# Performance work log

Measured on AMD Instinct MI355X. Metric: run time of the kernel, lower is better.

The kernel has to match this reference:

```python
import jax, jax.numpy as jnp
import numpy as np

B, N = 8192, 4096
OUT_DIM = 32


def setup_inputs() -> dict:
    key = jax.random.key(0)
    k_rr, k_drop, k_w1, k_b1, k_w2, k_b2 = jax.random.split(key, 6)
    rr = jax.random.uniform(k_rr, (B, N), dtype=jnp.float32, minval=0.4, maxval=1.4)
    drop = jax.random.uniform(k_drop, (B, N)) < 0.3
    rr = jnp.where(drop, 0.0, rr)
    # projection MLP params (Linear(6,16) -> ReLU -> Dropout(eval: identity) -> Linear(16,32))
    w1 = jax.random.normal(k_w1, (6, 16), dtype=jnp.float32) * (1.0 / np.sqrt(6))
    b1 = jax.random.normal(k_b1, (16,), dtype=jnp.float32) * 0.01
    w2 = jax.random.normal(k_w2, (16, OUT_DIM), dtype=jnp.float32) * (1.0 / np.sqrt(16))
    b2 = jax.random.normal(k_b2, (OUT_DIM,), dtype=jnp.float32) * 0.01
    return {"rr_intervals": rr, "w1": w1, "b1": b1, "w2": w2, "b2": b2}


def _hrv_features(rr):
    # rr: (B, N) float32, zero-padded. Faithful to the per-row torch loop, vectorized.
    dt = rr.dtype
    mask = rr > 0                                   # (B, N)
    cnt = jnp.sum(mask, axis=1)                     # (B,) int
    cntf = cnt.astype(dt)
    # masked mean / unbiased std (torch.std default ddof=1)
    denom_m = jnp.maximum(cntf, 1.0)
    mean_rr = jnp.sum(jnp.where(mask, rr, 0.0), axis=1) / denom_m
    dev = jnp.where(mask, rr - mean_rr[:, None], 0.0)
    var = jnp.sum(dev * dev, axis=1) / jnp.maximum(cntf - 1.0, 1.0)
    sdnn = jnp.sqrt(var)
    # compact valid entries to the front (stable -> preserves order), so diffs
    # match torch.diff(rr[rr > 0])
    order = jnp.argsort(jnp.logical_not(mask), axis=1, stable=True)  # (B, N)
    compact = jnp.take_along_axis(rr, order, axis=1)                  # (B, N)
    diffs = compact[:, 1:] - compact[:, :-1]                          # (B, N-1)
    dmask = jnp.arange(N - 1)[None, :] < (cnt - 1)[:, None]           # valid diffs
    ndiff = jnp.maximum(cntf - 1.0, 1.0)
    rmssd = jnp.sqrt(jnp.sum(jnp.where(dmask, diffs * diffs, 0.0), axis=1) / ndiff)
    nn50 = jnp.sum(((jnp.abs(diffs) > 0.05) & dmask).astype(dt), axis=1)
    pnn50 = nn50 / ndiff
    hr = 60.0 / jnp.maximum(mean_rr, 1e-12)
    cv = sdnn / jnp.maximum(mean_rr, 1e-12)
    feats = jnp.stack([mean_rr, sdnn, rmssd, pnn50, hr, cv], axis=1)  # (B, 6)
    feats = jnp.where((cnt > 1)[:, None], feats, 0.0)
    # per-column batch normalization, applied only where column max > 0
    col_max = jnp.max(feats, axis=0)
    col_mean = jnp.mean(feats, axis=0)
    col_std = jnp.std(feats, axis=0, ddof=1)
    normed = (feats - col_mean[None, :]) / (col_std[None, :] + 1e-8)
    feats = jnp.where((col_max > 0)[None, :], normed, feats)
    return feats


def reference(rr_intervals, w1, b1, w2, b2):
    feats = _hrv_features(rr_intervals)                 # (B, 6)
    h = jax.nn.relu(feats @ w1 + b1)                    # (B, 16); dropout in eval = identity
    return h @ w2 + b2                                  # (B, OUT_DIM)
```

## Files before the change

kernel.cpp:

```cpp
#include <hip/hip_runtime.h>
#include <math.h>

#define BATCH 8192
#define NLEN 4096

__global__ __launch_bounds__(256) void hrv_feats_kernel(
    const float* __restrict__ rr, float* __restrict__ feats) {
    const int lane = threadIdx.x & 63;
    const int wid = threadIdx.x >> 6;
    const int row = blockIdx.x * 4 + wid;
    const float* r = rr + (size_t)row * NLEN + lane * 64;

    double dsum = 0.0, dsumsq = 0.0, dsumd2 = 0.0;
    int cnt = 0, nn50 = 0;
    float prev = 0.f, first = 0.f;
    bool has = false;

    float x[32];
    float4* xv = reinterpret_cast<float4*>(x);
    const float4* rv = reinterpret_cast<const float4*>(r);

#pragma unroll
    for (int half = 0; half < 2; ++half) {
#pragma unroll
        for (int i = 0; i < 8; ++i) xv[i] = rv[half * 8 + i];
#pragma unroll
        for (int c = 0; c < 2; ++c) {
            float s = 0.f, s2 = 0.f, d2 = 0.f;
#pragma unroll
            for (int i = 0; i < 16; ++i) {
                const float v = x[c * 16 + i];
                const bool valid = v > 0.f;
                s += v;
                s2 = fmaf(v, v, s2);
                cnt += valid ? 1 : 0;
                const float d = v - prev;
                const float dm = (valid && has) ? d : 0.f;
                d2 = fmaf(dm, dm, d2);
                nn50 += (fabsf(dm) > 0.05f) ? 1 : 0;
                first = (valid && !has) ? v : first;
                prev = valid ? v : prev;
                has = has || valid;
            }
            dsum += s;
            dsumsq += s2;
            dsumd2 += d2;
        }
    }

    unsigned long long m = __ballot(has);
    unsigned long long pm = m & ((1ull << lane) - 1ull);
    int j = 63 - __clzll(pm | 1ull);
    float lastj = __shfl(prev, j, 64);
    if (has && pm) {
        float d = first - lastj;
        dsumd2 += (double)(d * d);
        nn50 += (fabsf(d) > 0.05f) ? 1 : 0;
    }

#pragma unroll
    for (int off = 32; off; off >>= 1) {
        dsum += __shfl_xor(dsum, off, 64);
        dsumsq += __shfl_xor(dsumsq, off, 64);
        dsumd2 += __shfl_xor(dsumd2, off, 64);
        cnt += __shfl_xor(cnt, off, 64);
        nn50 += __shfl_xor(nn50, off, 64);
    }

    const float cntf = (float)cnt;
    const float denom_m = fmaxf(cntf, 1.f);
    const float mean = (float)(dsum / (double)denom_m);
    const float varsum = (float)(dsumsq - (double)cnt * (double)mean * (double)mean);
    const float denom_v = fmaxf(cntf - 1.f, 1.f);
    const float sdnn = sqrtf(fmaxf(varsum / denom_v, 0.f));
    const float rmssd = sqrtf(fmaxf((float)(dsumd2 / (double)denom_v), 0.f));
    const float pnn50 = (float)nn50 / denom_v;
    const float hr = 60.f / fmaxf(mean, 1e-12f);
    const float cv = sdnn / fmaxf(mean, 1e-12f);

    float val = mean;
    val = (lane == 1) ? sdnn : val;
    val = (lane == 2) ? rmssd : val;
    val = (lane == 3) ? pnn50 : val;
    val = (lane == 4) ? hr : val;
    val = (lane == 5) ? cv : val;
    if (cnt <= 1) val = 0.f;
    if (lane < 6) feats[lane * BATCH + row] = val;
}

__global__ __launch_bounds__(256) void stats_mlp_kernel(
    const float* __restrict__ feats,
    const float* __restrict__ w1, const float* __restrict__ b1,
    const float* __restrict__ w2, const float* __restrict__ b2,
    float* __restrict__ out) {
    __shared__ double sh_s[4][6], sh_s2[4][6];
    __shared__ float sh_m[4][6];
    __shared__ float sh_stats[18];

    const int t = threadIdx.x;
    double s[6], s2[6];
    float mx[6];
#pragma unroll
    for (int c = 0; c < 6; ++c) { s[c] = 0.0; s2[c] = 0.0; mx[c] = -INFINITY; }

#pragma unroll
    for (int c = 0; c < 6; ++c) {
        const float4* col = reinterpret_cast<const float4*>(feats + c * BATCH);
#pragma unroll
        for (int it = 0; it < BATCH / 4 / 256; ++it) {
            float4 f4 = col[t + it * 256];
            const float f[4] = {f4.x, f4.y, f4.z, f4.w};
#pragma unroll
            for (int k = 0; k < 4; ++k) {
                s[c] += (double)f[k];
                s2[c] += (double)f[k] * (double)f[k];
                mx[c] = fmaxf(mx[c], f[k]);
            }
        }
    }
#pragma unroll
    for (int off = 32; off; off >>= 1) {
#pragma unroll
        for (int c = 0; c < 6; ++c) {
            s[c] += __shfl_down(s[c], off, 64);
            s2[c] += __shfl_down(s2[c], off, 64);
            mx[c] = fmaxf(mx[c], __shfl_down(mx[c], off, 64));
        }
    }
    if ((t & 63) == 0) {
        const int w = t >> 6;
#pragma unroll
        for (int c = 0; c < 6; ++c) {
            sh_s[w][c] = s[c];
            sh_s2[w][c] = s2[c];
            sh_m[w][c] = mx[c];
        }
    }
    __syncthreads();
    if (t < 6) {
        double S = 0, S2 = 0;
        float M = -INFINITY;
        for (int w = 0; w < 4; ++w) {
            S += sh_s[w][t];
            S2 += sh_s2[w][t];
            M = fmaxf(M, sh_m[w][t]);
        }
        const double meanb = S / (double)BATCH;
        double var = (S2 - (double)BATCH * meanb * meanb) / (double)(BATCH - 1);
        if (var < 0.0) var = 0.0;
        sh_stats[t] = (float)meanb;
        sh_stats[6 + t] = (float)sqrt(var);
        sh_stats[12 + t] = M;
    }
    __syncthreads();

    const int row = blockIdx.x * 256 + t;
    float f[6];
#pragma unroll
    for (int c = 0; c < 6; ++c) {
        float v = feats[c * BATCH + row];
        if (sh_stats[12 + c] > 0.f) v = (v - sh_stats[c]) / (sh_stats[6 + c] + 1e-8f);
        f[c] = v;
    }
    float h[16];
#pragma unroll
    for (int j = 0; j < 16; ++j) {
        float a = b1[j];
#pragma unroll
        for (int c = 0; c < 6; ++c) a = fmaf(f[c], w1[c * 16 + j], a);
        h[j] = fmaxf(a, 0.f);
    }
    float o[32];
#pragma unroll
    for (int k = 0; k < 32; ++k) o[k] = b2[k];
#pragma unroll
    for (int j = 0; j < 16; ++j) {
        const float hj = h[j];
#pragma unroll
        for (int k = 0; k < 32; ++k) o[k] = fmaf(hj, w2[j * 32 + k], o[k]);
    }
    float4* ov = reinterpret_cast<float4*>(out + (size_t)row * 32);
    const float4* op = reinterpret_cast<const float4*>(o);
#pragma unroll
    for (int i = 0; i < 8; ++i) ov[i] = op[i];
}

extern "C" void kernel_launch(void* const* d_in, const int* in_sizes, int n_in,
                              void* d_out, int out_size, void* d_ws, size_t ws_size,
                              hipStream_t stream) {
    const float* rr = (const float*)d_in[0];
    const float* w1 = (const float*)d_in[1];
    const float* b1 = (const float*)d_in[2];
    const float* w2 = (const float*)d_in[3];
    const float* b2 = (const float*)d_in[4];
    float* out = (float*)d_out;
    float* feats = (float*)d_ws;

    hrv_feats_kernel<<<BATCH / 4, 256, 0, stream>>>(rr, feats);
    stats_mlp_kernel<<<BATCH / 256, 256, 0, stream>>>(feats, w1, b1, w2, b2, out);
}
```

Measured before the change: 42.54 us.

## Coalesce row loads by interleaving float4 chunks across lanes with segmented boundary handling

Each lane now reads 16 float4 chunks strided by 256 floats, so one wavefront instruction covers a contiguous 1 KB span. Before, each lane owned a contiguous 64-float segment, which gave strided, poorly coalesced accesses. Because order now interleaves across lanes, each group resolves its cross-lane boundary diffs with ballot/shuffle. Group-level first/last values are combined in a sequential pass, which adds many shuffles and ballots per group.

```diff
diff --git a/kernel.cpp b/kernel.cpp
--- a/kernel.cpp
+++ b/kernel.cpp
@@ -9,53 +9,70 @@
     const int lane = threadIdx.x & 63;
     const int wid = threadIdx.x >> 6;
     const int row = blockIdx.x * 4 + wid;
-    const float* r = rr + (size_t)row * NLEN + lane * 64;
+    const float* rbase = rr + (size_t)row * NLEN + lane * 4;
+
+    float4 v4[16];
+#pragma unroll
+    for (int g = 0; g < 16; ++g)
+        v4[g] = *reinterpret_cast<const float4*>(rbase + g * 256);
 
     double dsum = 0.0, dsumsq = 0.0, dsumd2 = 0.0;
     int cnt = 0, nn50 = 0;
-    float prev = 0.f, first = 0.f;
-    bool has = false;
-
-    float x[32];
-    float4* xv = reinterpret_cast<float4*>(x);
-    const float4* rv = reinterpret_cast<const float4*>(r);
-
-#pragma unroll
-    for (int half = 0; half < 2; ++half) {
-#pragma unroll
-        for (int i = 0; i < 8; ++i) xv[i] = rv[half * 8 + i];
-#pragma unroll
-        for (int c = 0; c < 2; ++c) {
-            float s = 0.f, s2 = 0.f, d2 = 0.f;
-#pragma unroll
-            for (int i = 0; i < 16; ++i) {
-                const float v = x[c * 16 + i];
-                const bool valid = v > 0.f;
-                s += v;
-                s2 = fmaf(v, v, s2);
-                cnt += valid ? 1 : 0;
-                const float d = v - prev;
-                const float dm = (valid && has) ? d : 0.f;
-                d2 = fmaf(dm, dm, d2);
-                nn50 += (fabsf(dm) > 0.05f) ? 1 : 0;
-                first = (valid && !has) ? v : first;
-                prev = valid ? v : prev;
-                has = has || valid;
-            }
-            dsum += s;
-            dsumsq += s2;
-            dsumd2 += d2;
-        }
-    }
-
-    unsigned long long m = __ballot(has);
-    unsigned long long pm = m & ((1ull << lane) - 1ull);
-    int j = 63 - __clzll(pm | 1ull);
-    float lastj = __shfl(prev, j, 64);
-    if (has && pm) {
-        float d = first - lastj;
-        dsumd2 += (double)(d * d);
-        nn50 += (fabsf(d) > 0.05f) ? 1 : 0;
+    float fg[16], lg[16];
+    unsigned int hasbits = 0;
+
+    float s = 0.f, s2 = 0.f, d2 = 0.f;
+#pragma unroll
+    for (int g = 0; g < 16; ++g) {
+        const float xx[4] = {v4[g].x, v4[g].y, v4[g].z, v4[g].w};
+        float prev = 0.f, first = 0.f;
+        bool has = false;
+#pragma unroll
+        for (int k = 0; k < 4; ++k) {
+            const float v = xx[k];
+            const bool val = v > 0.f;
+            s += v;
+            s2 = fmaf(v, v, s2);
+            cnt += val ? 1 : 0;
+            const float d = v - prev;
+            const float dm = (val && has) ? d : 0.f;
+            d2 = fmaf(dm, dm, d2);
+            nn50 += (fabsf(dm) > 0.05f) ? 1 : 0;
+            first = (val && !has) ? v : first;
+            prev = val ? v : prev;
+            has = has || val;
+        }
+        const unsigned long long m = __ballot(has);
+        const unsigned long long pm = m & ((1ull << lane) - 1ull);
+        const int j = 63 - __clzll(pm | 1ull);
+        const float lastj = __shfl(prev, j, 64);
+        const float dB = first - lastj;
+        const float dBm = (has && pm) ? dB : 0.f;
+        d2 = fmaf(dBm, dBm, d2);
+        nn50 += (fabsf(dBm) > 0.05f) ? 1 : 0;
+        const int hi = 63 - __clzll(m | 1ull);
+        const int lo = (m != 0ull) ? (__ffsll((unsigned long long)m) - 1) : 0;
+        lg[g] = __shfl(prev, hi, 64);
+        fg[g] = __shfl(first, lo, 64);
+        hasbits |= (m != 0ull) ? (1u << g) : 0u;
+
+        if ((g & 3) == 3) {
+            dsum += s; dsumsq += s2; dsumd2 += d2;
+            s = 0.f; s2 = 0.f; d2 = 0.f;
+        }
+    }
+
+    float run_last = 0.f, sd2 = 0.f;
+    int run_has = 0, snn = 0;
+#pragma unroll
+    for (int g = 0; g < 16; ++g) {
+        const int hg = (hasbits >> g) & 1;
+        const float d = fg[g] - run_last;
+        const float dm = (hg && run_has) ? d : 0.f;
+        sd2 = fmaf(dm, dm, sd2);
+        snn += (fabsf(dm) > 0.05f) ? 1 : 0;
+        run_last = hg ? lg[g] : run_last;
+        run_has |= hg;
     }
 
 #pragma unroll
@@ -66,6 +83,8 @@
         cnt += __shfl_xor(cnt, off, 64);
         nn50 += __shfl_xor(nn50, off, 64);
     }
+    dsumd2 += (double)sd2;
+    nn50 += snn;
 
     const float cntf = (float)cnt;
     const float denom_m = fmaxf(cntf, 1.f);
```

Measured after the change: 44.61 us. 1.05x slower.
